# Kernel tuning notes

Measured on AMD Instinct MI355X. Metric: run time of the kernel, lower is better.

Reference implementation:

```python
import jax, jax.numpy as jnp
import numpy as np

HIDDEN = 1024
NUM_HEADS = 16
HEAD_DIM = HIDDEN // NUM_HEADS  # 64
B, S = 2, 2048


def setup_inputs() -> dict:
    key = jax.random.key(0)
    ks = jax.random.split(key, 10)
    sd = 1.0 / np.sqrt(HIDDEN)
    x = jax.random.normal(ks[0], (B, S, HIDDEN), dtype=jnp.float32)
    # per-head projections stacked over head axis: [H, hidden, head_dim]
    Wq = jax.random.normal(ks[1], (NUM_HEADS, HIDDEN, HEAD_DIM), dtype=jnp.float32) * sd
    Wk = jax.random.normal(ks[2], (NUM_HEADS, HIDDEN, HEAD_DIM), dtype=jnp.float32) * sd
    Wv = jax.random.normal(ks[3], (NUM_HEADS, HIDDEN, HEAD_DIM), dtype=jnp.float32) * sd
    bq = jax.random.normal(ks[4], (NUM_HEADS, HEAD_DIM), dtype=jnp.float32) * sd
    bk = jax.random.normal(ks[5], (NUM_HEADS, HEAD_DIM), dtype=jnp.float32) * sd
    bv = jax.random.normal(ks[6], (NUM_HEADS, HEAD_DIM), dtype=jnp.float32) * sd
    # output projection: [all_head_size, hidden]
    Wo = jax.random.normal(ks[7], (HIDDEN, HIDDEN), dtype=jnp.float32) * sd
    bo = jax.random.normal(ks[8], (HIDDEN,), dtype=jnp.float32) * sd
    return {"x": x, "Wq": Wq, "bq": bq, "Wk": Wk, "bk": bk,
            "Wv": Wv, "bv": bv, "Wo": Wo, "bo": bo}


def reference(x, Wq, bq, Wk, bk, Wv, bv, Wo, bo):
    # Fused-across-heads equivalent of the per-head Python loop.
    # q,k,v: [B, H, S, Dh]
    q = jnp.einsum('bsd,hde->bhse', x, Wq) + bq[None, :, None, :]
    k = jnp.einsum('bsd,hde->bhse', x, Wk) + bk[None, :, None, :]
    v = jnp.einsum('bsd,hde->bhse', x, Wv) + bv[None, :, None, :]
    scale = 1.0 / jnp.sqrt(jnp.asarray(HEAD_DIM, dtype=x.dtype))
    scores = jnp.einsum('bhse,bhte->bhst', q, k) * scale  # [B,H,S,S]
    probs = jax.nn.softmax(scores, axis=-1)               # dropout=0 (eval)
    ctx = jnp.einsum('bhst,bhte->bhse', probs, v)         # [B,H,S,Dh]
    # concat heads on last dim (head order matches torch.cat over heads)
    ctx = jnp.transpose(ctx, (0, 2, 1, 3)).reshape(x.shape[0], x.shape[1], -1)
    out = ctx @ Wo + bo                                   # output projection
    return out
```

## Files before the change

kernel.cpp:

```cpp
#include <hip/hip_runtime.h>
#include <cstdint>

typedef unsigned short u16;
typedef __attribute__((ext_vector_type(8))) short short8;
typedef __attribute__((ext_vector_type(4))) short short4v;
typedef __attribute__((ext_vector_type(4))) float f32x4;
typedef __attribute__((ext_vector_type(4))) unsigned short u16x4;

__device__ __forceinline__ u16 f2bf(float x) {
    unsigned int u = __float_as_uint(x);
    u += 0x7fffu + ((u >> 16) & 1u);
    return (u16)(u >> 16);
}

__device__ __forceinline__ float fexp2(float x) {
#if __has_builtin(__builtin_amdgcn_exp2f)
    return __builtin_amdgcn_exp2f(x);
#else
    return exp2f(x);
#endif
}

__device__ __forceinline__ unsigned pack_bf16(float a, float b) {
    unsigned ua = __float_as_uint(a) + 0x8000u;
    unsigned ub = __float_as_uint(b) + 0x8000u;
    return __builtin_amdgcn_perm(ub, ua, 0x07060302u);
}

#if __has_builtin(__builtin_amdgcn_mfma_f32_16x16x16bf16_1k)
__device__ __forceinline__ f32x4 mfma16(short4v a, short4v b, f32x4 c) {
    return __builtin_amdgcn_mfma_f32_16x16x16bf16_1k(a, b, c, 0, 0, 0);
}
#else
__device__ __forceinline__ f32x4 mfma16(short4v a, short4v b, f32x4 c) {
    short8 a8 = {a[0], a[1], a[2], a[3], 0, 0, 0, 0};
    short8 b8 = {b[0], b[1], b[2], b[3], 0, 0, 0, 0};
    return __builtin_amdgcn_mfma_f32_16x16x32_bf16(a8, b8, c, 0, 0, 0);
}
#endif

__device__ __forceinline__ void gload_lds16(const u16* g, u16* l) {
    __builtin_amdgcn_global_load_lds(
        (const __attribute__((address_space(1))) void*)(g),
        (__attribute__((address_space(3))) void*)(l),
        16, 0, 0);
}

#define SBAR() do { __builtin_amdgcn_sched_barrier(0); \
                    __builtin_amdgcn_s_barrier(); \
                    __builtin_amdgcn_sched_barrier(0); } while (0)

__global__ __launch_bounds__(256) void prep_kernel(
    const float* __restrict__ x,
    const float* __restrict__ Wq, const float* __restrict__ Wk,
    const float* __restrict__ Wv, const float* __restrict__ Wo,
    u16* __restrict__ xb, u16* __restrict__ wqkv, u16* __restrict__ wot)
{
    __shared__ u16 tile[64][65];
    const int z = blockIdx.z;
    const int tc = threadIdx.x & 63, tr = threadIdx.x >> 6;

    if (z == 1) {
        const int blk = blockIdx.y * 16 + blockIdx.x;
        const int base = (blk * 256 + threadIdx.x) * 4;
        #pragma unroll
        for (int i = 0; i < 16; ++i) {
            const int idx = base + i * 262144;
            float4 v = *(const float4*)(x + idx);
            u16x4 o;
            o.x = f2bf(v.x); o.y = f2bf(v.y); o.z = f2bf(v.z); o.w = f2bf(v.w);
            *(u16x4*)(xb + idx) = o;
        }
        return;
    }

    const float* src;
    u16* dst;
    int C, R, rb, cb;
    if (z == 0) {
        src = Wo; dst = wot; C = 1024; R = 1024;
        rb = blockIdx.x * 64; cb = blockIdx.y * 64;
    } else {
        const float* W = (z == 2) ? Wq : (z == 3) ? Wk : Wv;
        const int head = blockIdx.y;
        src = W + head * 65536;
        dst = wqkv + (size_t)(z - 2) * 1048576 + head * 65536;
        C = 64; R = 1024;
        rb = blockIdx.x * 64; cb = 0;
    }
    #pragma unroll
    for (int i = 0; i < 64; i += 4)
        tile[tr + i][tc] = f2bf(src[(size_t)(rb + tr + i) * C + (cb + tc)]);
    __syncthreads();
    #pragma unroll
    for (int i = 0; i < 64; i += 4)
        dst[(size_t)(cb + tr + i) * R + (rb + tc)] = tile[tc][tr + i];
}

__global__ __launch_bounds__(512, 2) void gemm_qkv_kernel(
    const u16* __restrict__ X, const u16* __restrict__ W,
    const float* __restrict__ bq, const float* __restrict__ bk,
    const float* __restrict__ bv,
    u16* __restrict__ qo, u16* __restrict__ ko, u16* __restrict__ vto)
{
    __shared__ __align__(16) u16 lds[65536];
    const int tid = threadIdx.x;
    const int lane = tid & 63;
    const int wid = tid >> 6;
    const int wm = wid >> 2;
    const int wn = wid & 3;
    const int c = lane & 15, qd = lane >> 4;

    const int id = (blockIdx.x & 7) * 24 + (blockIdx.x >> 3);
    const int m0 = (id / 12) * 256;
    const int n0 = (id % 12) * 256;
    const u16* Xb = X + (size_t)m0 * 1024;
    const u16* Wb = W + (size_t)n0 * 1024;

    const int scg  = (tid & 7) ^ ((tid >> 3) & 7);
    const int srow = tid >> 3;
    const int co0 = (qd ^ (c & 7)) * 8;
    const int co1 = ((4 + qd) ^ (c & 7)) * 8;
    const int rA = wm * 128 + c;
    const int rB = wn * 64 + c;

    auto stageA = [&](int t, int qa) {
        const int pb = (t & 1) * 32768;
        gload_lds16(Xb + (size_t)(qa * 64 + srow) * 1024 + t * 64 + scg * 8,
                    &lds[pb + (qa * 512 + tid) * 8]);
    };
    auto stageB = [&](int t, int qb) {
        const int pb = (t & 1) * 32768;
        gload_lds16(Wb + (size_t)(qb * 64 + srow) * 1024 + t * 64 + scg * 8,
                    &lds[pb + 16384 + (qb * 512 + tid) * 8]);
    };

    f32x4 acc[8][4];
    #pragma unroll
    for (int mi = 0; mi < 8; ++mi)
        #pragma unroll
        for (int ni = 0; ni < 4; ++ni) acc[mi][ni] = f32x4{0.f, 0.f, 0.f, 0.f};

    #pragma unroll
    for (int q = 0; q < 4; ++q) stageA(0, q);
    #pragma unroll
    for (int q = 0; q < 4; ++q) stageB(0, q);
    #pragma unroll
    for (int q = 0; q < 4; ++q) stageA(1, q);
    #pragma unroll
    for (int q = 0; q < 4; ++q) stageB(1, q);
    __builtin_amdgcn_s_waitcnt(0xF78);
    SBAR();

    #pragma unroll 2
    for (int t = 0; t < 16; ++t) {
        const int pb = (t & 1) * 32768;
        const u16* Al = &lds[pb];
        const u16* Bl = &lds[pb + 16384];

        short8 af0[4][2], bf0[2][2];
        #pragma unroll
        for (int mi = 0; mi < 4; ++mi) {
            af0[mi][0] = *(const short8*)&Al[(rA + mi * 16) * 64 + co0];
            af0[mi][1] = *(const short8*)&Al[(rA + mi * 16) * 64 + co1];
        }
        #pragma unroll
        for (int ni = 0; ni < 2; ++ni) {
            bf0[ni][0] = *(const short8*)&Bl[(rB + ni * 16) * 64 + co0];
            bf0[ni][1] = *(const short8*)&Bl[(rB + ni * 16) * 64 + co1];
        }
        SBAR();
        __builtin_amdgcn_s_setprio(1);
        #pragma unroll
        for (int mi = 0; mi < 4; ++mi)
            #pragma unroll
            for (int ni = 0; ni < 2; ++ni) {
                acc[mi][ni] = __builtin_amdgcn_mfma_f32_16x16x32_bf16(af0[mi][0], bf0[ni][0], acc[mi][ni], 0, 0, 0);
                acc[mi][ni] = __builtin_amdgcn_mfma_f32_16x16x32_bf16(af0[mi][1], bf0[ni][1], acc[mi][ni], 0, 0, 0);
            }
        __builtin_amdgcn_s_setprio(0);
        SBAR();

        short8 bf1[2][2];
        #pragma unroll
        for (int ni = 0; ni < 2; ++ni) {
            bf1[ni][0] = *(const short8*)&Bl[(rB + (ni + 2) * 16) * 64 + co0];
            bf1[ni][1] = *(const short8*)&Bl[(rB + (ni + 2) * 16) * 64 + co1];
        }
        if (t < 14) { stageA(t + 2, 0); stageA(t + 2, 2); }
        SBAR();
        __builtin_amdgcn_s_setprio(1);
        #pragma unroll
        for (int mi = 0; mi < 4; ++mi)
            #pragma unroll
            for (int ni = 0; ni < 2; ++ni) {
                acc[mi][ni + 2] = __builtin_amdgcn_mfma_f32_16x16x32_bf16(af0[mi][0], bf1[ni][0], acc[mi][ni + 2], 0, 0, 0);
                acc[mi][ni + 2] = __builtin_amdgcn_mfma_f32_16x16x32_bf16(af0[mi][1], bf1[ni][1], acc[mi][ni + 2], 0, 0, 0);
            }
        __builtin_amdgcn_s_setprio(0);
        SBAR();

        short8 af1[4][2];
        #pragma unroll
        for (int mi = 0; mi < 4; ++mi) {
            af1[mi][0] = *(const short8*)&Al[(rA + (mi + 4) * 16) * 64 + co0];
            af1[mi][1] = *(const short8*)&Al[(rA + (mi + 4) * 16) * 64 + co1];
        }
        if (t < 14) { stageB(t + 2, 0); stageB(t + 2, 1); stageB(t + 2, 2); stageB(t + 2, 3); }
        SBAR();
        __builtin_amdgcn_s_setprio(1);
        #pragma unroll
        for (int mi = 0; mi < 4; ++mi)
            #pragma unroll
            for (int ni = 0; ni < 2; ++ni) {
                acc[mi + 4][ni + 2] = __builtin_amdgcn_mfma_f32_16x16x32_bf16(af1[mi][0], bf1[ni][0], acc[mi + 4][ni + 2], 0, 0, 0);
                acc[mi + 4][ni + 2] = __builtin_amdgcn_mfma_f32_16x16x32_bf16(af1[mi][1], bf1[ni][1], acc[mi + 4][ni + 2], 0, 0, 0);
            }
        __builtin_amdgcn_s_setprio(0);
        SBAR();

        if (t < 14) { stageA(t + 2, 1); stageA(t + 2, 3); }
        SBAR();
        __builtin_amdgcn_s_setprio(1);
        #pragma unroll
        for (int mi = 0; mi < 4; ++mi)
            #pragma unroll
            for (int ni = 0; ni < 2; ++ni) {
                acc[mi + 4][ni] = __builtin_amdgcn_mfma_f32_16x16x32_bf16(af1[mi][0], bf0[ni][0], acc[mi + 4][ni], 0, 0, 0);
                acc[mi + 4][ni] = __builtin_amdgcn_mfma_f32_16x16x32_bf16(af1[mi][1], bf0[ni][1], acc[mi + 4][ni], 0, 0, 0);
            }
        __builtin_amdgcn_s_setprio(0);
        if (t < 14)       __builtin_amdgcn_s_waitcnt(0xF78);
        else if (t == 14) __builtin_amdgcn_s_waitcnt(0xF70);
        SBAR();
    }

    #pragma unroll
    for (int mi = 0; mi < 8; ++mi) {
        const int mbase = m0 + wm * 128 + mi * 16 + qd * 4;
        const int b = mbase >> 11;
        #pragma unroll
        for (int ni = 0; ni < 4; ++ni) {
            const int n = n0 + wn * 64 + ni * 16 + c;
            const int mat = n >> 10;
            const int idx = n & 1023;
            const int h = idx >> 6, e = idx & 63;
            const float bias = (mat == 0 ? bq : (mat == 1 ? bk : bv))[idx];
            if (mat == 2) {
                const int s = mbase & 2047;
                u16x4 pv;
                pv.x = f2bf(acc[mi][ni][0] + bias);
                pv.y = f2bf(acc[mi][ni][1] + bias);
                pv.z = f2bf(acc[mi][ni][2] + bias);
                pv.w = f2bf(acc[mi][ni][3] + bias);
                *(u16x4*)(vto + ((((size_t)(b * 16 + h) * 128 + (s >> 4)) * 64 + e) * 16
                                 + (s & 15))) = pv;
            } else {
                const float scale = (mat == 0) ? 0.18033688011112042f : 1.0f;
                u16* dst = (mat == 0) ? qo : ko;
                #pragma unroll
                for (int r = 0; r < 4; ++r) {
                    const int s = (mbase + r) & 2047;
                    dst[((size_t)((b * 16 + h) * 2048 + s)) * 64 + e] =
                        f2bf((acc[mi][ni][r] + bias) * scale);
                }
            }
        }
    }
}

__global__ __launch_bounds__(256, 3) void flash_kernel(
    const u16* __restrict__ Q,
    const u16* __restrict__ K,
    const u16* __restrict__ V2,
    u16* __restrict__ ctx)
{
    __shared__ __align__(16) char pool[34816];
    u16* stage = (u16*)pool;
    float (*Os)[64][66] = (float (*)[64][66])pool;
    float (*Ls)[64] = (float (*)[64])(pool + 33792);

    const int tid = threadIdx.x, lane = tid & 63, w = tid >> 6;
    const int c = lane & 15, qd = lane >> 4;
    const int bid = blockIdx.x;
    const int r5 = bid & 31;
    const int bh = (r5 & 7) * 4 + (r5 >> 3);
    const int q0 = (bid >> 5) * 64;
    const int b = bh >> 4, h = bh & 15;
    const u16* Qh = Q + (size_t)bh * 2048 * 64;
    const u16* Kh = K + (size_t)bh * 2048 * 64;
    const u16* Vh = V2 + (size_t)bh * 128 * 1024;

    u16* Kst = stage + w * 3072;

    const int krow8 = lane >> 3;
    const int kgc = (lane & 7) ^ (krow8 & 7);
    const int voff = c * 16 + qd * 4;

    short8 qf[4][2];
    #pragma unroll
    for (int qb = 0; qb < 4; ++qb)
        #pragma unroll
        for (int kb = 0; kb < 2; ++kb)
            qf[qb][kb] = *(const short8*)&Qh[(size_t)(q0 + qb * 16 + c) * 64 + kb * 32 + qd * 8];

    f32x4 o[4][4];
    float lsum[4];
    #pragma unroll
    for (int mt = 0; mt < 4; ++mt)
        #pragma unroll
        for (int qb = 0; qb < 4; ++qb) o[mt][qb] = f32x4{0.f, 0.f, 0.f, 0.f};
    #pragma unroll
    for (int qb = 0; qb < 4; ++qb) lsum[qb] = 0.f;

    #pragma unroll
    for (int j = 0; j < 2; ++j) {
        const int row = j * 8 + krow8;
        gload_lds16(Kh + (size_t)(w * 512 + row) * 64 + kgc * 8,
                    Kst + j * 512 + lane * 8);
    }
    short4v vA[4], vB[4];
    {
        const u16* vb = Vh + (size_t)(w * 32) * 1024 + voff;
        #pragma unroll
        for (int mt = 0; mt < 4; ++mt)
            vA[mt] = *(const short4v*)(vb + mt * 256);
    }
    #pragma unroll
    for (int j = 0; j < 2; ++j) {
        const int row = j * 8 + krow8;
        gload_lds16(Kh + (size_t)(w * 512 + 16 + row) * 64 + kgc * 8,
                    Kst + 1024 + j * 512 + lane * 8);
    }

    int cur = 0;
    auto body = [&](int it, short4v (&VC)[4], short4v (&VN)[4]) {
        u16* Kb = Kst + cur * 1024;

        __builtin_amdgcn_s_waitcnt(0xF74);
        __builtin_amdgcn_sched_barrier(0);

        short8 kf[2];
        #pragma unroll
        for (int kb = 0; kb < 2; ++kb)
            kf[kb] = *(const short8*)&Kb[c * 64 + ((4 * kb + qd) ^ (c & 7)) * 8];

        __builtin_amdgcn_sched_barrier(0);

        {
            const int itn = (it + 1) & 31;
            const u16* vb = Vh + (size_t)(w * 32 + itn) * 1024 + voff;
            #pragma unroll
            for (int mt = 0; mt < 4; ++mt)
                VN[mt] = *(const short4v*)(vb + mt * 256);
        }
        {
            const int itn = (it + 2) & 31;
            const int t0n = w * 512 + itn * 16;
            const int nslot = (cur >= 1) ? cur - 1 : 2;
            u16* Kn = Kst + nslot * 1024;
            #pragma unroll
            for (int j = 0; j < 2; ++j) {
                const int row = j * 8 + krow8;
                gload_lds16(Kh + (size_t)(t0n + row) * 64 + kgc * 8,
                            Kn + j * 512 + lane * 8);
            }
        }

        f32x4 sc[4];
        #pragma unroll
        for (int qb = 0; qb < 4; ++qb) {
            sc[qb] = f32x4{0.f, 0.f, 0.f, 0.f};
            sc[qb] = __builtin_amdgcn_mfma_f32_16x16x32_bf16(kf[0], qf[qb][0], sc[qb], 0, 0, 0);
            sc[qb] = __builtin_amdgcn_mfma_f32_16x16x32_bf16(kf[1], qf[qb][1], sc[qb], 0, 0, 0);
        }

        short4v pb[4];
        #pragma unroll
        for (int qb = 0; qb < 4; ++qb) {
            float p0 = fexp2(sc[qb][0]);
            float p1 = fexp2(sc[qb][1]);
            float p2 = fexp2(sc[qb][2]);
            float p3 = fexp2(sc[qb][3]);
            lsum[qb] += (p0 + p1) + (p2 + p3);
            unsigned d0 = pack_bf16(p0, p1);
            unsigned d1 = pack_bf16(p2, p3);
            union { unsigned u[2]; short4v s; } pu;
            pu.u[0] = d0; pu.u[1] = d1;
            pb[qb] = pu.s;
        }

        #pragma unroll
        for (int qb = 0; qb < 4; ++qb)
            #pragma unroll
            for (int mt = 0; mt < 4; ++mt)
                o[mt][qb] = mfma16(VC[mt], pb[qb], o[mt][qb]);

        cur = (cur == 2) ? 0 : cur + 1;
    };

    for (int it2 = 0; it2 < 16; ++it2) {
        body(2 * it2, vA, vB);
        body(2 * it2 + 1, vB, vA);
    }

    __builtin_amdgcn_s_waitcnt(0xF70);
    __syncthreads();

    #pragma unroll
    for (int qb = 0; qb < 4; ++qb) {
        lsum[qb] += __shfl_xor(lsum[qb], 16, 64);
        lsum[qb] += __shfl_xor(lsum[qb], 32, 64);
    }
    if (qd == 0) {
        #pragma unroll
        for (int qb = 0; qb < 4; ++qb) Ls[w][qb * 16 + c] = lsum[qb];
    }

    if (w >= 2) {
        float (*S)[66] = Os[w - 2];
        #pragma unroll
        for (int mt = 0; mt < 4; ++mt)
            #pragma unroll
            for (int qb = 0; qb < 4; ++qb)
                #pragma unroll
                for (int r = 0; r < 4; ++r)
                    S[mt * 16 + qd * 4 + r][qb * 16 + c] = o[mt][qb][r];
    }
    __syncthreads();
    if (w < 2) {
        float (*S)[66] = Os[w];
        #pragma unroll
        for (int mt = 0; mt < 4; ++mt)
            #pragma unroll
            for (int qb = 0; qb < 4; ++qb)
                #pragma unroll
                for (int r = 0; r < 4; ++r)
                    o[mt][qb][r] += S[mt * 16 + qd * 4 + r][qb * 16 + c];
    }
    __syncthreads();
    if (w == 1) {
        float (*S)[66] = Os[0];
        #pragma unroll
        for (int mt = 0; mt < 4; ++mt)
            #pragma unroll
            for (int qb = 0; qb < 4; ++qb)
                #pragma unroll
                for (int r = 0; r < 4; ++r)
                    S[mt * 16 + qd * 4 + r][qb * 16 + c] = o[mt][qb][r];
    }
    __syncthreads();
    if (w == 0) {
        float (*S)[66] = Os[0];
        float inv[4];
        #pragma unroll
        for (int qb = 0; qb < 4; ++qb) {
            int q = qb * 16 + c;
            float l = (Ls[0][q] + Ls[1][q]) + (Ls[2][q] + Ls[3][q]);
            inv[qb] = __builtin_amdgcn_rcpf(l);
        }
        #pragma unroll
        for (int mt = 0; mt < 4; ++mt)
            #pragma unroll
            for (int qb = 0; qb < 4; ++qb) {
                u16x4 ov;
                #pragma unroll
                for (int r = 0; r < 4; ++r) {
                    float v = (o[mt][qb][r] + S[mt * 16 + qd * 4 + r][qb * 16 + c]) * inv[qb];
                    ((u16*)&ov)[r] = f2bf(v);
                }
                *(u16x4*)&ctx[((size_t)(b * 2048 + q0 + qb * 16 + c)) * 1024
                              + h * 64 + mt * 16 + qd * 4] = ov;
            }
    }
}

__global__ __launch_bounds__(256, 4) void gemm_out_kernel(
    const u16* __restrict__ A, const u16* __restrict__ Wt,
    const float* __restrict__ bo, float* __restrict__ out)
{
    __shared__ __align__(16) u16 As[64 * 32];
    __shared__ __align__(16) u16 Bs[128 * 32];
    const int tid = threadIdx.x;
    const int lane = tid & 63;
    const int wv = tid >> 6;
    const int wm = wv & 1, wn = wv >> 1;
    const int m0 = blockIdx.x * 64;
    const int n0 = blockIdx.y * 128;
    const int c = lane & 15, qd = lane >> 4;

    f32x4 acc[2][4];
    #pragma unroll
    for (int a = 0; a < 2; ++a)
        #pragma unroll
        for (int b2 = 0; b2 < 4; ++b2) acc[a][b2] = f32x4{0.f, 0.f, 0.f, 0.f};

    const u16* Ab = A + (size_t)m0 * 1024;
    const u16* Wb = Wt + (size_t)n0 * 1024;

    for (int kt = 0; kt < 1024; kt += 32) {
        {
            int row = tid >> 2, part = tid & 3;
            gload_lds16(Ab + (size_t)row * 1024 + kt + part * 8, &As[tid * 8]);
        }
        #pragma unroll
        for (int i = 0; i < 2; ++i) {
            int slot = i * 256 + tid;
            int row = slot >> 2, part = slot & 3;
            gload_lds16(Wb + (size_t)row * 1024 + kt + part * 8, &Bs[slot * 8]);
        }
        __syncthreads();
        short8 af[2], bf[4];
        #pragma unroll
        for (int mt = 0; mt < 2; ++mt)
            af[mt] = *(const short8*)&As[(wm * 32 + mt * 16 + c) * 32 + qd * 8];
        #pragma unroll
        for (int nt = 0; nt < 4; ++nt)
            bf[nt] = *(const short8*)&Bs[(wn * 64 + nt * 16 + c) * 32 + qd * 8];
        #pragma unroll
        for (int mt = 0; mt < 2; ++mt)
            #pragma unroll
            for (int nt = 0; nt < 4; ++nt)
                acc[mt][nt] = __builtin_amdgcn_mfma_f32_16x16x32_bf16(af[mt], bf[nt], acc[mt][nt], 0, 0, 0);
        __syncthreads();
    }

    #pragma unroll
    for (int mt = 0; mt < 2; ++mt) {
        const int mbase = m0 + wm * 32 + mt * 16 + qd * 4;
        #pragma unroll
        for (int nt = 0; nt < 4; ++nt) {
            const int n = n0 + wn * 64 + nt * 16 + c;
            const float bias = bo[n];
            #pragma unroll
            for (int r = 0; r < 4; ++r)
                out[(size_t)(mbase + r) * 1024 + n] = acc[mt][nt][r] + bias;
        }
    }
}

extern "C" void kernel_launch(void* const* d_in, const int* in_sizes, int n_in,
                              void* d_out, int out_size, void* d_ws, size_t ws_size,
                              hipStream_t stream) {
    const float* x  = (const float*)d_in[0];
    const float* Wq = (const float*)d_in[1];
    const float* bq = (const float*)d_in[2];
    const float* Wk = (const float*)d_in[3];
    const float* bk = (const float*)d_in[4];
    const float* Wv = (const float*)d_in[5];
    const float* bv = (const float*)d_in[6];
    const float* Wo = (const float*)d_in[7];
    const float* bo = (const float*)d_in[8];
    float* out = (float*)d_out;

    u16* ws    = (u16*)d_ws;
    u16* xb    = ws;
    u16* wqkv  = xb + 4096 * 1024;
    u16* wot   = wqkv + 3072 * 1024;
    u16* qws   = wot + 1024 * 1024;
    u16* kws   = qws + 4194304;
    u16* v2ws  = kws + 4194304;
    u16* ctxws = v2ws + 4194304;

    prep_kernel<<<dim3(16, 16, 5), 256, 0, stream>>>(x, Wq, Wk, Wv, Wo, xb, wqkv, wot);
    gemm_qkv_kernel<<<192, 512, 0, stream>>>(xb, wqkv, bq, bk, bv, qws, kws, v2ws);
    flash_kernel<<<1024, 256, 0, stream>>>(qws, kws, v2ws, ctxws);
    gemm_out_kernel<<<dim3(64, 8), 256, 0, stream>>>(ctxws, wot, bo, out);
}
```

Measured before the change: 190.7 us.

## Retile QKV GEMM to 256x192 tiles for a full 256-block grid

The QKV projection GEMM now uses 256x192 output tiles instead of 256x256. That gives 256 workgroups instead of 192, matching the 256 CUs on MI355X so no wave of blocks is left partially idle. The block-to-tile mapping, LDS buffer sizes, B-operand staging count, wait counts and the MFMA phase schedule are rewritten for three N-subtiles per wave, merging four compute phases into three. The trade-off is a lower compute-to-load ratio per tile and a reworked interleave of global loads and MFMAs, which could expose more memory latency.

```diff
diff --git a/kernel.cpp b/kernel.cpp
--- a/kernel.cpp
+++ b/kernel.cpp
@@ -103,7 +103,7 @@
     const float* __restrict__ bv,
     u16* __restrict__ qo, u16* __restrict__ ko, u16* __restrict__ vto)
 {
-    __shared__ __align__(16) u16 lds[65536];
+    __shared__ __align__(16) u16 lds[57344];
     const int tid = threadIdx.x;
     const int lane = tid & 63;
     const int wid = tid >> 6;
@@ -111,9 +111,9 @@
     const int wn = wid & 3;
     const int c = lane & 15, qd = lane >> 4;
 
-    const int id = (blockIdx.x & 7) * 24 + (blockIdx.x >> 3);
-    const int m0 = (id / 12) * 256;
-    const int n0 = (id % 12) * 256;
+    const int grp = blockIdx.x & 7, k = blockIdx.x >> 3;
+    const int m0 = ((grp >> 1) * 4 + (k >> 3)) * 256;
+    const int n0 = ((grp & 1) * 8 + (k & 7)) * 192;
     const u16* Xb = X + (size_t)m0 * 1024;
     const u16* Wb = W + (size_t)n0 * 1024;
 
@@ -122,43 +122,43 @@
     const int co0 = (qd ^ (c & 7)) * 8;
     const int co1 = ((4 + qd) ^ (c & 7)) * 8;
     const int rA = wm * 128 + c;
-    const int rB = wn * 64 + c;
+    const int rB = wn * 48 + c;
 
     auto stageA = [&](int t, int qa) {
-        const int pb = (t & 1) * 32768;
+        const int pb = (t & 1) * 28672;
         gload_lds16(Xb + (size_t)(qa * 64 + srow) * 1024 + t * 64 + scg * 8,
                     &lds[pb + (qa * 512 + tid) * 8]);
     };
     auto stageB = [&](int t, int qb) {
-        const int pb = (t & 1) * 32768;
+        const int pb = (t & 1) * 28672;
         gload_lds16(Wb + (size_t)(qb * 64 + srow) * 1024 + t * 64 + scg * 8,
                     &lds[pb + 16384 + (qb * 512 + tid) * 8]);
     };
 
-    f32x4 acc[8][4];
+    f32x4 acc[8][3];
     #pragma unroll
     for (int mi = 0; mi < 8; ++mi)
         #pragma unroll
-        for (int ni = 0; ni < 4; ++ni) acc[mi][ni] = f32x4{0.f, 0.f, 0.f, 0.f};
+        for (int ni = 0; ni < 3; ++ni) acc[mi][ni] = f32x4{0.f, 0.f, 0.f, 0.f};
 
     #pragma unroll
     for (int q = 0; q < 4; ++q) stageA(0, q);
     #pragma unroll
-    for (int q = 0; q < 4; ++q) stageB(0, q);
+    for (int q = 0; q < 3; ++q) stageB(0, q);
     #pragma unroll
     for (int q = 0; q < 4; ++q) stageA(1, q);
     #pragma unroll
-    for (int q = 0; q < 4; ++q) stageB(1, q);
-    __builtin_amdgcn_s_waitcnt(0xF78);
+    for (int q = 0; q < 3; ++q) stageB(1, q);
+    __builtin_amdgcn_s_waitcnt(0xF77);
     SBAR();
 
     #pragma unroll 2
     for (int t = 0; t < 16; ++t) {
-        const int pb = (t & 1) * 32768;
+        const int pb = (t & 1) * 28672;
         const u16* Al = &lds[pb];
         const u16* Bl = &lds[pb + 16384];
 
-        short8 af0[4][2], bf0[2][2];
+        short8 af0[4][2], bf[3][2];
         #pragma unroll
         for (int mi = 0; mi < 4; ++mi) {
             af0[mi][0] = *(const short8*)&Al[(rA + mi * 16) * 64 + co0];
@@ -166,8 +166,8 @@
         }
         #pragma unroll
         for (int ni = 0; ni < 2; ++ni) {
-            bf0[ni][0] = *(const short8*)&Bl[(rB + ni * 16) * 64 + co0];
-            bf0[ni][1] = *(const short8*)&Bl[(rB + ni * 16) * 64 + co1];
+            bf[ni][0] = *(const short8*)&Bl[(rB + ni * 16) * 64 + co0];
+            bf[ni][1] = *(const short8*)&Bl[(rB + ni * 16) * 64 + co1];
         }
         SBAR();
         __builtin_amdgcn_s_setprio(1);
@@ -175,62 +175,51 @@
         for (int mi = 0; mi < 4; ++mi)
             #pragma unroll
             for (int ni = 0; ni < 2; ++ni) {
-                acc[mi][ni] = __builtin_amdgcn_mfma_f32_16x16x32_bf16(af0[mi][0], bf0[ni][0], acc[mi][ni], 0, 0, 0);
-                acc[mi][ni] = __builtin_amdgcn_mfma_f32_16x16x32_bf16(af0[mi][1], bf0[ni][1], acc[mi][ni], 0, 0, 0);
+                acc[mi][ni] = __builtin_amdgcn_mfma_f32_16x16x32_bf16(af0[mi][0], bf[ni][0], acc[mi][ni], 0, 0, 0);
+                acc[mi][ni] = __builtin_amdgcn_mfma_f32_16x16x32_bf16(af0[mi][1], bf[ni][1], acc[mi][ni], 0, 0, 0);
             }
         __builtin_amdgcn_s_setprio(0);
         SBAR();
 
-        short8 bf1[2][2];
-        #pragma unroll
-        for (int ni = 0; ni < 2; ++ni) {
-            bf1[ni][0] = *(const short8*)&Bl[(rB + (ni + 2) * 16) * 64 + co0];
-            bf1[ni][1] = *(const short8*)&Bl[(rB + (ni + 2) * 16) * 64 + co1];
-        }
+        short8 af1[4][2];
+        #pragma unroll
+        for (int mi = 0; mi < 4; ++mi) {
+            af1[mi][0] = *(const short8*)&Al[(rA + (mi + 4) * 16) * 64 + co0];
+            af1[mi][1] = *(const short8*)&Al[(rA + (mi + 4) * 16) * 64 + co1];
+        }
+        bf[2][0] = *(const short8*)&Bl[(rB + 2 * 16) * 64 + co0];
+        bf[2][1] = *(const short8*)&Bl[(rB + 2 * 16) * 64 + co1];
         if (t < 14) { stageA(t + 2, 0); stageA(t + 2, 2); }
         SBAR();
         __builtin_amdgcn_s_setprio(1);
         #pragma unroll
+        for (int mi = 0; mi < 4; ++mi) {
+            acc[mi][2] = __builtin_amdgcn_mfma_f32_16x16x32_bf16(af0[mi][0], bf[2][0], acc[mi][2], 0, 0, 0);
+            acc[mi][2] = __builtin_amdgcn_mfma_f32_16x16x32_bf16(af0[mi][1], bf[2][1], acc[mi][2], 0, 0, 0);
+        }
+        #pragma unroll
+        for (int mi = 0; mi < 4; ++mi) {
+            acc[mi + 4][0] = __builtin_amdgcn_mfma_f32_16x16x32_bf16(af1[mi][0], bf[0][0], acc[mi + 4][0], 0, 0, 0);
+            acc[mi + 4][0] = __builtin_amdgcn_mfma_f32_16x16x32_bf16(af1[mi][1], bf[0][1], acc[mi + 4][0], 0, 0, 0);
+        }
+        __builtin_amdgcn_s_setprio(0);
+        SBAR();
+
+        if (t < 14) {
+            stageA(t + 2, 1); stageA(t + 2, 3);
+            stageB(t + 2, 0); stageB(t + 2, 1); stageB(t + 2, 2);
+        }
+        SBAR();
+        __builtin_amdgcn_s_setprio(1);
+        #pragma unroll
         for (int mi = 0; mi < 4; ++mi)
             #pragma unroll
-            for (int ni = 0; ni < 2; ++ni) {
-                acc[mi][ni + 2] = __builtin_amdgcn_mfma_f32_16x16x32_bf16(af0[mi][0], bf1[ni][0], acc[mi][ni + 2], 0, 0, 0);
-                acc[mi][ni + 2] = __builtin_amdgcn_mfma_f32_16x16x32_bf16(af0[mi][1], bf1[ni][1], acc[mi][ni + 2], 0, 0, 0);
+            for (int ni = 1; ni < 3; ++ni) {
+                acc[mi + 4][ni] = __builtin_amdgcn_mfma_f32_16x16x32_bf16(af1[mi][0], bf[ni][0], acc[mi + 4][ni], 0, 0, 0);
+                acc[mi + 4][ni] = __builtin_amdgcn_mfma_f32_16x16x32_bf16(af1[mi][1], bf[ni][1], acc[mi + 4][ni], 0, 0, 0);
             }
         __builtin_amdgcn_s_setprio(0);
-        SBAR();
-
-        short8 af1[4][2];
-        #pragma unroll
-        for (int mi = 0; mi < 4; ++mi) {
-            af1[mi][0] = *(const short8*)&Al[(rA + (mi + 4) * 16) * 64 + co0];
-            af1[mi][1] = *(const short8*)&Al[(rA + (mi + 4) * 16) * 64 + co1];
-        }
-        if (t < 14) { stageB(t + 2, 0); stageB(t + 2, 1); stageB(t + 2, 2); stageB(t + 2, 3); }
-        SBAR();
-        __builtin_amdgcn_s_setprio(1);
-        #pragma unroll
-        for (int mi = 0; mi < 4; ++mi)
-            #pragma unroll
-            for (int ni = 0; ni < 2; ++ni) {
-                acc[mi + 4][ni + 2] = __builtin_amdgcn_mfma_f32_16x16x32_bf16(af1[mi][0], bf1[ni][0], acc[mi + 4][ni + 2], 0, 0, 0);
-                acc[mi + 4][ni + 2] = __builtin_amdgcn_mfma_f32_16x16x32_bf16(af1[mi][1], bf1[ni][1], acc[mi + 4][ni + 2], 0, 0, 0);
-            }
-        __builtin_amdgcn_s_setprio(0);
-        SBAR();
-
-        if (t < 14) { stageA(t + 2, 1); stageA(t + 2, 3); }
-        SBAR();
-        __builtin_amdgcn_s_setprio(1);
-        #pragma unroll
-        for (int mi = 0; mi < 4; ++mi)
-            #pragma unroll
-            for (int ni = 0; ni < 2; ++ni) {
-                acc[mi + 4][ni] = __builtin_amdgcn_mfma_f32_16x16x32_bf16(af1[mi][0], bf0[ni][0], acc[mi + 4][ni], 0, 0, 0);
-                acc[mi + 4][ni] = __builtin_amdgcn_mfma_f32_16x16x32_bf16(af1[mi][1], bf0[ni][1], acc[mi + 4][ni], 0, 0, 0);
-            }
-        __builtin_amdgcn_s_setprio(0);
-        if (t < 14)       __builtin_amdgcn_s_waitcnt(0xF78);
+        if (t < 14)       __builtin_amdgcn_s_waitcnt(0xF77);
         else if (t == 14) __builtin_amdgcn_s_waitcnt(0xF70);
         SBAR();
     }
@@ -240,8 +229,8 @@
         const int mbase = m0 + wm * 128 + mi * 16 + qd * 4;
         const int b = mbase >> 11;
         #pragma unroll
-        for (int ni = 0; ni < 4; ++ni) {
-            const int n = n0 + wn * 64 + ni * 16 + c;
+        for (int ni = 0; ni < 3; ++ni) {
+            const int n = n0 + wn * 48 + ni * 16 + c;
             const int mat = n >> 10;
             const int idx = n & 1023;
             const int h = idx >> 6, e = idx & 63;
@@ -563,7 +552,7 @@
     u16* ctxws = v2ws + 4194304;
 
     prep_kernel<<<dim3(16, 16, 5), 256, 0, stream>>>(x, Wq, Wk, Wv, Wo, xb, wqkv, wot);
-    gemm_qkv_kernel<<<192, 512, 0, stream>>>(xb, wqkv, bq, bk, bv, qws, kws, v2ws);
+    gemm_qkv_kernel<<<256, 512, 0, stream>>>(xb, wqkv, bq, bk, bv, qws, kws, v2ws);
     flash_kernel<<<1024, 256, 0, stream>>>(qws, kws, v2ws, ctxws);
     gemm_out_kernel<<<dim3(64, 8), 256, 0, stream>>>(ctxws, wot, bo, out);
 }
```

After: 188.7 us. No clear change (-1.0%).
